# Performance work log

Measured on AMD Instinct MI355X. Metric: run time of the kernel, lower is better.

## Reference

```python
import jax, jax.numpy as jnp
import numpy as np

K, S, P = 3, 2, 2  # kernel_size, stride, padding (dilation=1)


def _unfold(xp, k, s, oh, ow):
    """Extract k*k strided patches from a padded array.

    xp: (..., Hp, Wp) -> (..., k*k, oh, ow), window-position ordering (kh, kw)
    matching torch.nn.Unfold (channel-major handled by caller).
    """
    return jnp.stack(
        [xp[..., i:i + s * (oh - 1) + 1:s, j:j + s * (ow - 1) + 1:s]
         for i in range(K) for j in range(K)],
        axis=-3,
    )


def setup_inputs() -> dict:
    key = jax.random.key(0)
    x = jax.random.normal(key, (8, 256, 128, 128), dtype=jnp.float32)
    return {"x": x}


def reference(x):
    b, c, h, w = x.shape
    oh = (h - K + 2 * P) // S + 1
    ow = (w - K + 2 * P) // S + 1

    # channel-wise L2 norm, computed BEFORE unfolding (padding contributes 0 either way)
    n = jnp.sqrt(jnp.sum(x * x, axis=1))            # (b, h, w)
    n_pad = jnp.pad(n, ((0, 0), (P, P), (P, P)))
    n_patch = _unfold(n_pad, K, S, oh, ow)          # (b, k*k, oh, ow)
    # weighting_fn = softmax over the k*k window positions (torch dim=1 of unfolded norm)
    wts = jax.nn.softmax(n_patch, axis=1)           # (b, k*k, oh, ow)

    x_pad = jnp.pad(x, ((0, 0), (0, 0), (P, P), (P, P)))
    x_patch = _unfold(x_pad, K, S, oh, ow)          # (b, c, k*k, oh, ow)

    # weighted sum over window positions
    return jnp.sum(wts[:, None] * x_patch, axis=2)  # (b, c, oh, ow)
```

## Files before the change

kernel.cpp:

```cpp
#include <hip/hip_runtime.h>
#include <math.h>

#define BATCH 8
#define CH    256
#define H     128
#define W     128
#define HW    (H * W)
#define OH    65
#define OW    65
#define NPIX  (OH * OW)
#define CSPLIT 4
#define CPW   (CH / CSPLIT / 4)

__global__ __launch_bounds__(256) void norm_kernel(const float4* __restrict__ x4,
                                                   float4* __restrict__ n4) {
    __shared__ float4 part[4][64];
    const int lane = threadIdx.x & 63;
    const int wv   = threadIdx.x >> 6;
    const int q    = blockIdx.x * 64 + lane;
    const int b    = (q * 4) >> 14;
    const int qin  = q - b * (HW / 4);

    const float4* p = x4 + (size_t)(b * CH + wv * 64) * (HW / 4) + qin;
    float4 acc = {0.f, 0.f, 0.f, 0.f};
    #pragma unroll 8
    for (int c = 0; c < 64; ++c) {
        float4 v = p[(size_t)c * (HW / 4)];
        acc.x += v.x * v.x; acc.y += v.y * v.y;
        acc.z += v.z * v.z; acc.w += v.w * v.w;
    }
    part[wv][lane] = acc;
    __syncthreads();
    if (wv == 0) {
        float4 a0 = part[0][lane], a1 = part[1][lane];
        float4 a2 = part[2][lane], a3 = part[3][lane];
        float4 r;
        r.x = sqrtf(a0.x + a1.x + a2.x + a3.x);
        r.y = sqrtf(a0.y + a1.y + a2.y + a3.y);
        r.z = sqrtf(a0.z + a1.z + a2.z + a3.z);
        r.w = sqrtf(a0.w + a1.w + a2.w + a3.w);
        n4[q] = r;
    }
}

__global__ __launch_bounds__(256) void pool_kernel(const float* __restrict__ x,
                                                   const float* __restrict__ n,
                                                   float* __restrict__ out) {
    __shared__ float wts[OW][9];
    const int oh = blockIdx.x;
    const int b  = blockIdx.y;
    const int z  = blockIdx.z;
    const int t  = threadIdx.x;

    if (t < OW) {
        const float* nb = n + b * HW;
        const int iw0 = 2 * t - 2;
        float ww[9];
        bool  vl[9];
        float m = 0.f;
        #pragma unroll
        for (int r = 0; r < 3; ++r) {
            int ih = 2 * oh + r - 2;
            bool vh = (unsigned)ih < (unsigned)H;
            int ihc = ih < 0 ? 0 : (ih > H - 1 ? H - 1 : ih);
            #pragma unroll
            for (int kw = 0; kw < 3; ++kw) {
                int iw = iw0 + kw;
                bool v = vh && ((unsigned)iw < (unsigned)W);
                int iwc = iw < 0 ? 0 : (iw > W - 1 ? W - 1 : iw);
                float nv = v ? nb[ihc * W + iwc] : 0.f;
                vl[r * 3 + kw] = v;
                ww[r * 3 + kw] = nv;
                m = fmaxf(m, nv);
            }
        }
        float d = 0.f;
        #pragma unroll
        for (int k = 0; k < 9; ++k) {
            float e = __expf(ww[k] - m);
            d += e;
            ww[k] = vl[k] ? e : 0.f;
        }
        float inv = 1.f / d;
        #pragma unroll
        for (int k = 0; k < 9; ++k) wts[t][k] = ww[k] * inv;
    }
    __syncthreads();

    const int lane = t & 63;
    const int wv   = t >> 6;

    float w0[9], w64[9];
    #pragma unroll
    for (int k = 0; k < 9; ++k) { w0[k] = wts[lane][k]; w64[k] = wts[OW - 1][k]; }

    int rb[3];
    #pragma unroll
    for (int r = 0; r < 3; ++r) {
        int ih = 2 * oh + r - 2;
        int ihc = ih < 0 ? 0 : (ih > H - 1 ? H - 1 : ih);
        rb[r] = ihc * W;
    }

    const int cbase = z * (CH / CSPLIT) + wv * CPW;
    const float* xb = x + (size_t)(b * CH + cbase) * HW;
    float*       ob = out + (size_t)(b * CH + cbase) * NPIX + oh * OW;

    #pragma unroll 4
    for (int c = 0; c < CPW; ++c) {
        const float* xc = xb + (size_t)c * HW;
        float2 own[3], prev[3];
        #pragma unroll
        for (int r = 0; r < 3; ++r)
            own[r] = *(const float2*)(xc + rb[r] + 2 * lane);
        #pragma unroll
        for (int r = 0; r < 3; ++r) {
            prev[r].x = __shfl_up(own[r].x, 1);
            prev[r].y = __shfl_up(own[r].y, 1);
        }
        float a0 = 0.f, a1 = 0.f;
        #pragma unroll
        for (int r = 0; r < 3; ++r) {
            a0 += w0[r * 3 + 0] * prev[r].x + w0[r * 3 + 1] * prev[r].y
                + w0[r * 3 + 2] * own[r].x;
            a1 += w64[r * 3 + 0] * own[r].x + w64[r * 3 + 1] * own[r].y;
        }
        float* oc = ob + (size_t)c * NPIX;
        oc[lane] = a0;
        if (lane == 63) oc[OW - 1] = a1;
    }
}

extern "C" void kernel_launch(void* const* d_in, const int* in_sizes, int n_in,
                              void* d_out, int out_size, void* d_ws, size_t ws_size,
                              hipStream_t stream) {
    const float* x = (const float*)d_in[0];
    float* out = (float*)d_out;
    float* nbuf = (float*)d_ws;

    norm_kernel<<<512, 256, 0, stream>>>((const float4*)x, (float4*)nbuf);

    dim3 grid(OH, BATCH, CSPLIT);
    pool_kernel<<<grid, 256, 0, stream>>>(x, nbuf, out);
}
```

Measured before the change: 239.7 us.

## Fuse norm and pooling into one cooperative kernel with grid sync

```diff
diff --git a/kernel.cpp b/kernel.cpp
--- a/kernel.cpp
+++ b/kernel.cpp
@@ -1,5 +1,8 @@
 #include <hip/hip_runtime.h>
+#include <hip/hip_cooperative_groups.h>
 #include <math.h>
+
+namespace cg = cooperative_groups;
 
 #define BATCH 8
 #define CH    256
@@ -11,123 +14,129 @@
 #define NPIX  (OH * OW)
 #define CSPLIT 4
 #define CPW   (CH / CSPLIT / 4)
+#define NORMBLK 512
+#define POOLUNITS (OH * BATCH * CSPLIT)
+#define GRID  1024
 
-__global__ __launch_bounds__(256) void norm_kernel(const float4* __restrict__ x4,
-                                                   float4* __restrict__ n4) {
+__global__ __launch_bounds__(256, 4) void fused_kernel(const float* __restrict__ x,
+                                                       float* __restrict__ nbuf,
+                                                       float* __restrict__ out) {
     __shared__ float4 part[4][64];
-    const int lane = threadIdx.x & 63;
-    const int wv   = threadIdx.x >> 6;
-    const int q    = blockIdx.x * 64 + lane;
-    const int b    = (q * 4) >> 14;
-    const int qin  = q - b * (HW / 4);
+    __shared__ float wts[OW][9];
+    const int t    = threadIdx.x;
+    const int lane = t & 63;
+    const int wv   = t >> 6;
 
-    const float4* p = x4 + (size_t)(b * CH + wv * 64) * (HW / 4) + qin;
-    float4 acc = {0.f, 0.f, 0.f, 0.f};
-    #pragma unroll 8
-    for (int c = 0; c < 64; ++c) {
-        float4 v = p[(size_t)c * (HW / 4)];
-        acc.x += v.x * v.x; acc.y += v.y * v.y;
-        acc.z += v.z * v.z; acc.w += v.w * v.w;
+    if (blockIdx.x < NORMBLK) {
+        const float4* x4 = (const float4*)x;
+        const int q   = blockIdx.x * 64 + lane;
+        const int b   = (q * 4) >> 14;
+        const int qin = q - b * (HW / 4);
+        const float4* p = x4 + (size_t)(b * CH + wv * 64) * (HW / 4) + qin;
+        float4 acc = {0.f, 0.f, 0.f, 0.f};
+        #pragma unroll 8
+        for (int c = 0; c < 64; ++c) {
+            float4 v = p[(size_t)c * (HW / 4)];
+            acc.x += v.x * v.x; acc.y += v.y * v.y;
+            acc.z += v.z * v.z; acc.w += v.w * v.w;
+        }
+        part[wv][lane] = acc;
+        __syncthreads();
+        if (wv == 0) {
+            float4 a0 = part[0][lane], a1 = part[1][lane];
+            float4 a2 = part[2][lane], a3 = part[3][lane];
+            float4 r;
+            r.x = sqrtf(a0.x + a1.x + a2.x + a3.x);
+            r.y = sqrtf(a0.y + a1.y + a2.y + a3.y);
+            r.z = sqrtf(a0.z + a1.z + a2.z + a3.z);
+            r.w = sqrtf(a0.w + a1.w + a2.w + a3.w);
+            ((float4*)nbuf)[q] = r;
+        }
     }
-    part[wv][lane] = acc;
-    __syncthreads();
-    if (wv == 0) {
-        float4 a0 = part[0][lane], a1 = part[1][lane];
-        float4 a2 = part[2][lane], a3 = part[3][lane];
-        float4 r;
-        r.x = sqrtf(a0.x + a1.x + a2.x + a3.x);
-        r.y = sqrtf(a0.y + a1.y + a2.y + a3.y);
-        r.z = sqrtf(a0.z + a1.z + a2.z + a3.z);
-        r.w = sqrtf(a0.w + a1.w + a2.w + a3.w);
-        n4[q] = r;
-    }
-}
 
-__global__ __launch_bounds__(256) void pool_kernel(const float* __restrict__ x,
-                                                   const float* __restrict__ n,
-                                                   float* __restrict__ out) {
-    __shared__ float wts[OW][9];
-    const int oh = blockIdx.x;
-    const int b  = blockIdx.y;
-    const int z  = blockIdx.z;
-    const int t  = threadIdx.x;
+    cg::this_grid().sync();
 
-    if (t < OW) {
-        const float* nb = n + b * HW;
-        const int iw0 = 2 * t - 2;
-        float ww[9];
-        bool  vl[9];
-        float m = 0.f;
+    for (int vb = blockIdx.x; vb < POOLUNITS; vb += GRID) {
+        const int z   = vb / (OH * BATCH);
+        const int rem = vb - z * (OH * BATCH);
+        const int b   = rem / OH;
+        const int oh  = rem - b * OH;
+
+        if (t < OW) {
+            const float* nb = nbuf + b * HW;
+            const int iw0 = 2 * t - 2;
+            float ww[9];
+            bool  vl[9];
+            float m = 0.f;
+            #pragma unroll
+            for (int r = 0; r < 3; ++r) {
+                int ih = 2 * oh + r - 2;
+                bool vh = (unsigned)ih < (unsigned)H;
+                int ihc = ih < 0 ? 0 : (ih > H - 1 ? H - 1 : ih);
+                #pragma unroll
+                for (int kw = 0; kw < 3; ++kw) {
+                    int iw = iw0 + kw;
+                    bool v = vh && ((unsigned)iw < (unsigned)W);
+                    int iwc = iw < 0 ? 0 : (iw > W - 1 ? W - 1 : iw);
+                    float nv = v ? nb[ihc * W + iwc] : 0.f;
+                    vl[r * 3 + kw] = v;
+                    ww[r * 3 + kw] = nv;
+                    m = fmaxf(m, nv);
+                }
+            }
+            float d = 0.f;
+            #pragma unroll
+            for (int k = 0; k < 9; ++k) {
+                float e = __expf(ww[k] - m);
+                d += e;
+                ww[k] = vl[k] ? e : 0.f;
+            }
+            float inv = 1.f / d;
+            #pragma unroll
+            for (int k = 0; k < 9; ++k) wts[t][k] = ww[k] * inv;
+        }
+        __syncthreads();
+
+        float w0[9], w64[9];
+        #pragma unroll
+        for (int k = 0; k < 9; ++k) { w0[k] = wts[lane][k]; w64[k] = wts[OW - 1][k]; }
+
+        int rb[3];
         #pragma unroll
         for (int r = 0; r < 3; ++r) {
             int ih = 2 * oh + r - 2;
-            bool vh = (unsigned)ih < (unsigned)H;
             int ihc = ih < 0 ? 0 : (ih > H - 1 ? H - 1 : ih);
+            rb[r] = ihc * W;
+        }
+
+        const int cbase = z * (CH / CSPLIT) + wv * CPW;
+        const float* xb = x + (size_t)(b * CH + cbase) * HW;
+        float*       ob = out + (size_t)(b * CH + cbase) * NPIX + oh * OW;
+
+        #pragma unroll 4
+        for (int c = 0; c < CPW; ++c) {
+            const float* xc = xb + (size_t)c * HW;
+            float2 own[3], prev[3];
             #pragma unroll
-            for (int kw = 0; kw < 3; ++kw) {
-                int iw = iw0 + kw;
-                bool v = vh && ((unsigned)iw < (unsigned)W);
-                int iwc = iw < 0 ? 0 : (iw > W - 1 ? W - 1 : iw);
-                float nv = v ? nb[ihc * W + iwc] : 0.f;
-                vl[r * 3 + kw] = v;
-                ww[r * 3 + kw] = nv;
-                m = fmaxf(m, nv);
+            for (int r = 0; r < 3; ++r)
+                own[r] = *(const float2*)(xc + rb[r] + 2 * lane);
+            #pragma unroll
+            for (int r = 0; r < 3; ++r) {
+                prev[r].x = __shfl_up(own[r].x, 1);
+                prev[r].y = __shfl_up(own[r].y, 1);
             }
+            float a0 = 0.f, a1 = 0.f;
+            #pragma unroll
+            for (int r = 0; r < 3; ++r) {
+                a0 += w0[r * 3 + 0] * prev[r].x + w0[r * 3 + 1] * prev[r].y
+                    + w0[r * 3 + 2] * own[r].x;
+                a1 += w64[r * 3 + 0] * own[r].x + w64[r * 3 + 1] * own[r].y;
+            }
+            float* oc = ob + (size_t)c * NPIX;
+            oc[lane] = a0;
+            if (lane == 63) oc[OW - 1] = a1;
         }
-        float d = 0.f;
-        #pragma unroll
-        for (int k = 0; k < 9; ++k) {
-            float e = __expf(ww[k] - m);
-            d += e;
-            ww[k] = vl[k] ? e : 0.f;
-        }
-        float inv = 1.f / d;
-        #pragma unroll
-        for (int k = 0; k < 9; ++k) wts[t][k] = ww[k] * inv;
-    }
-    __syncthreads();
-
-    const int lane = t & 63;
-    const int wv   = t >> 6;
-
-    float w0[9], w64[9];
-    #pragma unroll
-    for (int k = 0; k < 9; ++k) { w0[k] = wts[lane][k]; w64[k] = wts[OW - 1][k]; }
-
-    int rb[3];
-    #pragma unroll
-    for (int r = 0; r < 3; ++r) {
-        int ih = 2 * oh + r - 2;
-        int ihc = ih < 0 ? 0 : (ih > H - 1 ? H - 1 : ih);
-        rb[r] = ihc * W;
-    }
-
-    const int cbase = z * (CH / CSPLIT) + wv * CPW;
-    const float* xb = x + (size_t)(b * CH + cbase) * HW;
-    float*       ob = out + (size_t)(b * CH + cbase) * NPIX + oh * OW;
-
-    #pragma unroll 4
-    for (int c = 0; c < CPW; ++c) {
-        const float* xc = xb + (size_t)c * HW;
-        float2 own[3], prev[3];
-        #pragma unroll
-        for (int r = 0; r < 3; ++r)
-            own[r] = *(const float2*)(xc + rb[r] + 2 * lane);
-        #pragma unroll
-        for (int r = 0; r < 3; ++r) {
-            prev[r].x = __shfl_up(own[r].x, 1);
-            prev[r].y = __shfl_up(own[r].y, 1);
-        }
-        float a0 = 0.f, a1 = 0.f;
-        #pragma unroll
-        for (int r = 0; r < 3; ++r) {
-            a0 += w0[r * 3 + 0] * prev[r].x + w0[r * 3 + 1] * prev[r].y
-                + w0[r * 3 + 2] * own[r].x;
-            a1 += w64[r * 3 + 0] * own[r].x + w64[r * 3 + 1] * own[r].y;
-        }
-        float* oc = ob + (size_t)c * NPIX;
-        oc[lane] = a0;
-        if (lane == 63) oc[OW - 1] = a1;
+        __syncthreads();
     }
 }
 
@@ -135,11 +144,10 @@
                               void* d_out, int out_size, void* d_ws, size_t ws_size,
                               hipStream_t stream) {
     const float* x = (const float*)d_in[0];
-    float* out = (float*)d_out;
+    float* out  = (float*)d_out;
     float* nbuf = (float*)d_ws;
 
-    norm_kernel<<<512, 256, 0, stream>>>((const float4*)x, (float4*)nbuf);
-
-    dim3 grid(OH, BATCH, CSPLIT);
-    pool_kernel<<<grid, 256, 0, stream>>>(x, nbuf, out);
+    void* args[] = {(void*)&x, (void*)&nbuf, (void*)&out};
+    hipLaunchCooperativeKernel((const void*)fused_kernel, dim3(GRID), dim3(256),
+                               args, 0, stream);
 }
```

After: 367.2 us. 1.53x slower.

## Fuse channel-norm computation into pooling kernel with per-block row norms

Applied to the files above, without the earlier changes.

```diff
diff --git a/kernel.cpp b/kernel.cpp
--- a/kernel.cpp
+++ b/kernel.cpp
@@ -9,51 +9,37 @@
 #define OH    65
 #define OW    65
 #define NPIX  (OH * OW)
-#define CSPLIT 4
-#define CPW   (CH / CSPLIT / 4)
 
-__global__ __launch_bounds__(256) void norm_kernel(const float4* __restrict__ x4,
-                                                   float4* __restrict__ n4) {
-    __shared__ float4 part[4][64];
-    const int lane = threadIdx.x & 63;
-    const int wv   = threadIdx.x >> 6;
-    const int q    = blockIdx.x * 64 + lane;
-    const int b    = (q * 4) >> 14;
-    const int qin  = q - b * (HW / 4);
+__global__ __launch_bounds__(512, 4) void fused_kernel(const float* __restrict__ x,
+                                                       float* __restrict__ out) {
+    __shared__ float nrm[3][W];
+    __shared__ float wts[OW][9];
+    const int oh   = blockIdx.x;
+    const int b    = blockIdx.y;
+    const int t    = threadIdx.x;
+    const int lane = t & 63;
+    const int wv   = t >> 6;
 
-    const float4* p = x4 + (size_t)(b * CH + wv * 64) * (HW / 4) + qin;
-    float4 acc = {0.f, 0.f, 0.f, 0.f};
-    #pragma unroll 8
-    for (int c = 0; c < 64; ++c) {
-        float4 v = p[(size_t)c * (HW / 4)];
-        acc.x += v.x * v.x; acc.y += v.y * v.y;
-        acc.z += v.z * v.z; acc.w += v.w * v.w;
+    if (t < 3 * W) {
+        const int r   = t >> 7;
+        const int col = t & (W - 1);
+        const int ih  = 2 * oh + r - 2;
+        float s = 0.f;
+        if ((unsigned)ih < (unsigned)H) {
+            const float* p = x + (size_t)b * CH * HW + ih * W + col;
+            float acc = 0.f;
+            #pragma unroll 8
+            for (int c = 0; c < CH; ++c) {
+                float v = p[(size_t)c * HW];
+                acc += v * v;
+            }
+            s = sqrtf(acc);
+        }
+        nrm[r][col] = s;
     }
-    part[wv][lane] = acc;
     __syncthreads();
-    if (wv == 0) {
-        float4 a0 = part[0][lane], a1 = part[1][lane];
-        float4 a2 = part[2][lane], a3 = part[3][lane];
-        float4 r;
-        r.x = sqrtf(a0.x + a1.x + a2.x + a3.x);
-        r.y = sqrtf(a0.y + a1.y + a2.y + a3.y);
-        r.z = sqrtf(a0.z + a1.z + a2.z + a3.z);
-        r.w = sqrtf(a0.w + a1.w + a2.w + a3.w);
-        n4[q] = r;
-    }
-}
-
-__global__ __launch_bounds__(256) void pool_kernel(const float* __restrict__ x,
-                                                   const float* __restrict__ n,
-                                                   float* __restrict__ out) {
-    __shared__ float wts[OW][9];
-    const int oh = blockIdx.x;
-    const int b  = blockIdx.y;
-    const int z  = blockIdx.z;
-    const int t  = threadIdx.x;
 
     if (t < OW) {
-        const float* nb = n + b * HW;
         const int iw0 = 2 * t - 2;
         float ww[9];
         bool  vl[9];
@@ -62,13 +48,12 @@
         for (int r = 0; r < 3; ++r) {
             int ih = 2 * oh + r - 2;
             bool vh = (unsigned)ih < (unsigned)H;
-            int ihc = ih < 0 ? 0 : (ih > H - 1 ? H - 1 : ih);
             #pragma unroll
             for (int kw = 0; kw < 3; ++kw) {
                 int iw = iw0 + kw;
                 bool v = vh && ((unsigned)iw < (unsigned)W);
                 int iwc = iw < 0 ? 0 : (iw > W - 1 ? W - 1 : iw);
-                float nv = v ? nb[ihc * W + iwc] : 0.f;
+                float nv = v ? nrm[r][iwc] : 0.f;
                 vl[r * 3 + kw] = v;
                 ww[r * 3 + kw] = nv;
                 m = fmaxf(m, nv);
@@ -87,9 +72,6 @@
     }
     __syncthreads();
 
-    const int lane = t & 63;
-    const int wv   = t >> 6;
-
     float w0[9], w64[9];
     #pragma unroll
     for (int k = 0; k < 9; ++k) { w0[k] = wts[lane][k]; w64[k] = wts[OW - 1][k]; }
@@ -102,12 +84,11 @@
         rb[r] = ihc * W;
     }
 
-    const int cbase = z * (CH / CSPLIT) + wv * CPW;
-    const float* xb = x + (size_t)(b * CH + cbase) * HW;
-    float*       ob = out + (size_t)(b * CH + cbase) * NPIX + oh * OW;
+    const float* xb = x + (size_t)(b * CH + wv * 32) * HW;
+    float*       ob = out + (size_t)(b * CH + wv * 32) * NPIX + oh * OW;
 
     #pragma unroll 4
-    for (int c = 0; c < CPW; ++c) {
+    for (int c = 0; c < 32; ++c) {
         const float* xc = xb + (size_t)c * HW;
         float2 own[3], prev[3];
         #pragma unroll
@@ -136,10 +117,6 @@
                               hipStream_t stream) {
     const float* x = (const float*)d_in[0];
     float* out = (float*)d_out;
-    float* nbuf = (float*)d_ws;
-
-    norm_kernel<<<512, 256, 0, stream>>>((const float4*)x, (float4*)nbuf);
-
-    dim3 grid(OH, BATCH, CSPLIT);
-    pool_kernel<<<grid, 256, 0, stream>>>(x, nbuf, out);
+    dim3 grid(OH, BATCH);
+    fused_kernel<<<grid, 512, 0, stream>>>(x, out);
 }
```

Result: faster. 232.6 us (-2.9%).
